# Optimization experiments

Hardware: AMD Instinct MI355X
Metric: run time of the kernel (lower is better)

## Reference

```python
import jax, jax.numpy as jnp
import numpy as np

DIM = 1024
HEADS = 16
DIM_HEAD = 64
INNER = HEADS * DIM_HEAD  # 1024
SCALE = DIM_HEAD ** -0.5


def setup_inputs() -> dict:
    key = jax.random.key(0)
    ks = jax.random.split(key, 5)
    B, N = 4, 2048
    x = jax.random.normal(ks[0], (B, N, DIM), dtype=jnp.float32)
    # torch Linear weights are [out, in]; store transposed [in, out] for x @ W
    s = 1.0 / np.sqrt(DIM)
    Wq = jax.random.uniform(ks[1], (DIM, INNER), minval=-s, maxval=s, dtype=jnp.float32)
    Wkv = jax.random.uniform(ks[2], (DIM, 2 * INNER), minval=-s, maxval=s, dtype=jnp.float32)
    so = 1.0 / np.sqrt(INNER)
    Wo = jax.random.uniform(ks[3], (INNER, DIM), minval=-so, maxval=so, dtype=jnp.float32)
    bo = jax.random.uniform(ks[4], (DIM,), minval=-so, maxval=so, dtype=jnp.float32)
    return {"x": x, "Wq": Wq, "Wkv": Wkv, "Wo": Wo, "bo": bo}


def reference(x, Wq, Wkv, Wo, bo):
    B, N, _ = x.shape
    q = x @ Wq                      # [B, N, INNER]
    kv = x @ Wkv                    # [B, N, 2*INNER]
    k, v = jnp.split(kv, 2, axis=-1)

    def split_heads(t):
        return t.reshape(B, N, HEADS, DIM_HEAD).transpose(0, 2, 1, 3)  # [B,H,N,D]

    q, k, v = split_heads(q) * SCALE, split_heads(k), split_heads(v)
    sim = jnp.einsum('bhid,bhjd->bhij', q, k)  # [B,H,N,N]
    mask_value = -jnp.finfo(sim.dtype).max
    # causal: mask strictly-upper triangle (triu with offset j-i+1 = 1)
    causal_mask = jnp.triu(jnp.ones((N, N), dtype=bool), k=1)
    sim = jnp.where(causal_mask[None, None, :, :], mask_value, sim)
    attn = jax.nn.softmax(sim, axis=-1)
    out = jnp.einsum('bhij,bhjd->bhid', attn, v)            # [B,H,N,D]
    out = out.transpose(0, 2, 1, 3).reshape(B, N, INNER)    # [B,N,INNER]
    return out @ Wo + bo
```

## Files before the change

kernel.cpp:

```cpp
#include <hip/hip_runtime.h>

typedef unsigned short u16;
typedef __bf16 bf16x8 __attribute__((ext_vector_type(8)));
typedef float floatx4 __attribute__((ext_vector_type(4)));
typedef unsigned as1_u32 __attribute__((address_space(1)));
typedef unsigned as3_u32 __attribute__((address_space(3)));

__device__ inline u16 f2bf(float f) {
    unsigned int u = __builtin_bit_cast(unsigned int, f);
    u += 0x7fffu + ((u >> 16) & 1u);
    return (u16)(u >> 16);
}
__device__ inline floatx4 mfma16(bf16x8 a, bf16x8 b, floatx4 c) {
    return __builtin_amdgcn_mfma_f32_16x16x32_bf16(a, b, c, 0, 0, 0);
}
__device__ inline void gld16(const u16* g, u16* l) {
    __builtin_amdgcn_global_load_lds((const as1_u32*)g, (as3_u32*)l, 16, 0, 0);
}
__device__ inline unsigned permpack(float lo, float hi) {
    return __builtin_amdgcn_perm(__builtin_bit_cast(unsigned, hi),
                                 __builtin_bit_cast(unsigned, lo), 0x07060302u);
}

#define NSEQ 2048
#define DIM  1024
#define HEADS 16
#define DHEAD 64
#define QSCALE 0.18033688f
#define CSHIFT 4.328085f

__device__ inline void transpose_tile(const float* __restrict__ src,
                                      u16* __restrict__ dst, int ncols,
                                      int n0, int k0, int t) {
    __shared__ u16 tile[64][72];
    #pragma unroll
    for (int rr = 0; rr < 4; rr++) {
        const int k = (t >> 4) + rr * 16;
        const int n = (t & 15) * 4;
        float4 v = *(const float4*)&src[(size_t)(k0 + k) * ncols + n0 + n];
        tile[n + 0][k] = f2bf(v.x); tile[n + 1][k] = f2bf(v.y);
        tile[n + 2][k] = f2bf(v.z); tile[n + 3][k] = f2bf(v.w);
    }
    __syncthreads();
    #pragma unroll
    for (int ww = 0; ww < 2; ww++) {
        const int idx = t + ww * 256;
        const int n = idx >> 3, g = idx & 7;
        u16 tmp[8] __attribute__((aligned(16)));
        #pragma unroll
        for (int i = 0; i < 8; i++) tmp[i] = tile[n][g * 8 + i];
        *(uint4*)&dst[(size_t)(n0 + n) * 1024 + k0 + g * 8] = *(const uint4*)tmp;
    }
}

__global__ __launch_bounds__(256) void prep_fused(
    const float* __restrict__ x,  u16* __restrict__ xb,
    const float* __restrict__ Wq, const float* __restrict__ Wkv,
    u16* __restrict__ Wt)
{
    const int bid = blockIdx.x;
    const int t = threadIdx.x;
    if (bid < 4096) {
        const size_t i = ((size_t)bid * 256 + t) * 8;
        float4 a = *(const float4*)&x[i];
        float4 b = *(const float4*)&x[i + 4];
        u16 o[8] __attribute__((aligned(16)));
        o[0] = f2bf(a.x); o[1] = f2bf(a.y); o[2] = f2bf(a.z); o[3] = f2bf(a.w);
        o[4] = f2bf(b.x); o[5] = f2bf(b.y); o[6] = f2bf(b.z); o[7] = f2bf(b.w);
        *(uint4*)&xb[i] = *(const uint4*)o;
    } else if (bid < 4352) {
        const int v = bid - 4096;
        transpose_tile(Wq, Wt, 1024, (v & 15) * 64, (v >> 4) * 64, t);
    } else {
        const int v = bid - 4352;
        transpose_tile(Wkv, Wt + (size_t)1024 * 1024, 2048, (v & 31) * 64, (v >> 5) * 64, t);
    }
}

__global__ __launch_bounds__(256) void transpose_conv(const float* __restrict__ src,
                                                      u16* __restrict__ dst, int ncols) {
    transpose_tile(src, dst, ncols, blockIdx.x * 64, blockIdx.y * 64, threadIdx.x);
}

__global__ __launch_bounds__(512, 2) void qkv_gemm_v4(
    const u16* __restrict__ xb, const u16* __restrict__ Wt,
    u16* __restrict__ q_ws, u16* __restrict__ k_ws, u16* __restrict__ v_ws)
{
    __shared__ u16 As[3][256 * 64];
    __shared__ u16 Bs[3][128 * 64];

    const int n0 = blockIdx.x * 128;
    const int m0 = blockIdx.y * 256;
    const int t = threadIdx.x, lane = t & 63, w = t >> 6;
    const int wr = w >> 1, wc = w & 1;
    const int quad = lane >> 4, l16 = lane & 15;

    const int srow = lane >> 3;
    const int c8   = (lane & 7) ^ srow;
    const size_t gA = (size_t)(m0 + w * 8 + srow) * DIM + c8 * 8;
    const size_t gB = (size_t)(n0 + w * 8 + srow) * DIM + c8 * 8;

    floatx4 acc[4][4];
    #pragma unroll
    for (int i = 0; i < 4; i++)
        #pragma unroll
        for (int j = 0; j < 4; j++) acc[i][j] = floatx4{0.f, 0.f, 0.f, 0.f};

#define STAGE_QKV(tt, buf) do {                                            \
    const size_t k0s = (size_t)(tt) * 64;                                  \
    u16* ab = &As[buf][w * 512];                                           \
    u16* bb = &Bs[buf][w * 512];                                           \
    gld16(&xb[gA + k0s],             ab);                                  \
    gld16(&xb[gA + k0s +  64 * DIM], ab + 4096);                           \
    gld16(&xb[gA + k0s + 128 * DIM], ab + 8192);                           \
    gld16(&xb[gA + k0s + 192 * DIM], ab + 12288);                          \
    gld16(&Wt[gB + k0s],             bb);                                  \
    gld16(&Wt[gB + k0s +  64 * DIM], bb + 4096);                           \
} while (0)

    STAGE_QKV(0, 0);
    STAGE_QKV(1, 1);

    int cur = 0, nxt = 2;
    for (int tt = 0; tt < 16; tt++) {
        __builtin_amdgcn_sched_barrier(0);
        __builtin_amdgcn_s_barrier();
        __builtin_amdgcn_sched_barrier(0);
        if (tt < 14) STAGE_QKV(tt + 2, nxt);
        __builtin_amdgcn_sched_barrier(0);
        if (tt < 14)       asm volatile("s_waitcnt vmcnt(12)" ::: "memory");
        else if (tt == 14) asm volatile("s_waitcnt vmcnt(6)"  ::: "memory");
        else               asm volatile("s_waitcnt vmcnt(0)"  ::: "memory");
        __builtin_amdgcn_sched_barrier(0);
        __builtin_amdgcn_s_barrier();
        __builtin_amdgcn_sched_barrier(0);

        const u16* al = &As[cur][0];
        const u16* bl = &Bs[cur][0];
        #pragma unroll
        for (int ks = 0; ks < 2; ks++) {
            bf16x8 af[4], bf[4];
            #pragma unroll
            for (int mi = 0; mi < 4; mi++)
                af[mi] = *(const bf16x8*)&al[(wr * 64 + mi * 16 + l16) * 64
                                             + (((ks * 4 + quad) ^ (l16 & 7)) * 8)];
            #pragma unroll
            for (int nj = 0; nj < 4; nj++)
                bf[nj] = *(const bf16x8*)&bl[(wc * 64 + nj * 16 + l16) * 64
                                             + (((ks * 4 + quad) ^ (l16 & 7)) * 8)];
            __builtin_amdgcn_s_setprio(1);
            #pragma unroll
            for (int mi = 0; mi < 4; mi++)
                #pragma unroll
                for (int nj = 0; nj < 4; nj++)
                    acc[mi][nj] = mfma16(af[mi], bf[nj], acc[mi][nj]);
            __builtin_amdgcn_s_setprio(0);
        }
        cur = (cur == 2) ? 0 : cur + 1;
        nxt = (nxt == 2) ? 0 : nxt + 1;
    }
#undef STAGE_QKV

    const int seg = n0 >> 10;
    #pragma unroll
    for (int nj = 0; nj < 4; nj++) {
        const int n  = n0 + wc * 64 + nj * 16 + l16;
        const int nn = n & 1023;
        const int h  = nn >> 6, d = nn & 63;
        #pragma unroll
        for (int mi = 0; mi < 4; mi++) {
            const int mb = m0 + wr * 64 + mi * 16 + quad * 4;
            const int b = mb >> 11, ib = mb & (NSEQ - 1);
            if (seg == 0) {
                #pragma unroll
                for (int r = 0; r < 4; r++)
                    q_ws[(((size_t)(b * HEADS + h)) * NSEQ + ib + r) * DHEAD + d] =
                        f2bf(acc[mi][nj][r] * QSCALE);
            } else if (seg == 1) {
                #pragma unroll
                for (int r = 0; r < 4; r++)
                    k_ws[(((size_t)(b * HEADS + h)) * NSEQ + ib + r) * DHEAD + d] =
                        f2bf(acc[mi][nj][r]);
            } else {
                u16 tmp[4] __attribute__((aligned(8)));
                #pragma unroll
                for (int r = 0; r < 4; r++) tmp[r] = f2bf(acc[mi][nj][r]);
                *(uint2*)&v_ws[(((size_t)(b * HEADS + h)) * DHEAD + d) * NSEQ + ib] =
                    *(const uint2*)tmp;
            }
        }
    }
}

__global__ __launch_bounds__(256) void attn_v8(
    const u16* __restrict__ q_ws, const u16* __restrict__ k_ws,
    const u16* __restrict__ v_ws, u16* __restrict__ attn_ws)
{
    __shared__ u16 kds[2][64 * 64];
    __shared__ u16 vds[2][64 * 64];
    __shared__ u16 p_lds[4 * 2048];

    const int bid = blockIdx.x;
    const int bh  = bid & 63;
    const int t16 = 15 - (bid >> 6);
    const int i0  = t16 * 128;
    const int b   = bh >> 4, h = bh & 15;

    const u16* qb = q_ws + (size_t)bh * NSEQ * DHEAD;
    const u16* kb = k_ws + (size_t)bh * NSEQ * DHEAD;
    const u16* vb = v_ws + (size_t)bh * DHEAD * NSEQ;

    const int t    = threadIdx.x;
    const int lane = t & 63, w = t >> 6;
    const int quad = lane >> 4, l16 = lane & 15;

    const int srow8 = lane >> 3;
    const int chunk = (lane & 7) ^ srow8;
    const int krow  = w * 16 + srow8;
    const size_t koff = (size_t)krow * DHEAD + chunk * 8;
    const size_t voff = (size_t)krow * NSEQ + chunk * 8;
    u16* klbase = (u16*)&kds[0][0] + w * 1024;
    u16* vlbase = (u16*)&vds[0][0] + w * 1024;
    const int sw = (l16 & 7);

    bf16x8 qf[2][2];
    #pragma unroll
    for (int rf = 0; rf < 2; rf++)
        #pragma unroll
        for (int dg = 0; dg < 2; dg++)
            qf[rf][dg] = *(const bf16x8*)&qb[(size_t)(i0 + rf * 64 + w * 16 + l16) * DHEAD
                                             + dg * 32 + quad * 8];

    floatx4 l4[2] = {floatx4{0.f,0.f,0.f,0.f}, floatx4{0.f,0.f,0.f,0.f}};
    floatx4 acc[2][4];
    #pragma unroll
    for (int rf = 0; rf < 2; rf++)
        #pragma unroll
        for (int dg = 0; dg < 4; dg++) acc[rf][dg] = floatx4{0.f, 0.f, 0.f, 0.f};

    const int jt_max = 2 * t16 + 1;

    gld16(&kb[koff],             klbase);
    gld16(&kb[koff + 8 * DHEAD], klbase + 512);
    gld16(&vb[voff],             vlbase);
    gld16(&vb[voff + 8 * NSEQ],  vlbase + 512);

    for (int jt = 0; jt <= jt_max; jt++) {
        const int cur = jt & 1;
        __syncthreads();

        if (jt < jt_max) {
            const size_t j64 = (size_t)(jt + 1) * 64;
            const int nb = (cur ^ 1) * 4096;
            gld16(&kb[j64 * DHEAD + koff],             klbase + nb);
            gld16(&kb[j64 * DHEAD + koff + 8 * DHEAD], klbase + nb + 512);
            gld16(&vb[j64 + voff],                     vlbase + nb);
            gld16(&vb[j64 + voff + 8 * NSEQ],          vlbase + nb + 512);
        }

        const u16* kl = &kds[cur][0];
        const u16* vl = &vds[cur][0];
        const int j0 = jt * 64;

        floatx4 s[2][4];
        #pragma unroll
        for (int rf = 0; rf < 2; rf++)
            #pragma unroll
            for (int g = 0; g < 4; g++)
                s[rf][g] = floatx4{-CSHIFT, -CSHIFT, -CSHIFT, -CSHIFT};
        __builtin_amdgcn_s_setprio(1);
        #pragma unroll
        for (int dg = 0; dg < 2; dg++)
            #pragma unroll
            for (int g = 0; g < 4; g++) {
                bf16x8 kf = *(const bf16x8*)&kl[(g * 16 + l16) * 64
                                                + (((dg * 4 + quad) ^ sw) * 8)];
                s[0][g] = mfma16(kf, qf[0][dg], s[0][g]);
                s[1][g] = mfma16(kf, qf[1][dg], s[1][g]);
            }
        __builtin_amdgcn_s_setprio(0);

        #pragma unroll
        for (int rf = 0; rf < 2; rf++) {
            const int imin = i0 + rf * 64 + w * 16;
            if (j0 + 63 > imin) {
                const int i = imin + l16;
                #pragma unroll
                for (int g = 0; g < 4; g++) {
                    const int jb = j0 + g * 16 + quad * 4;
                    #pragma unroll
                    for (int r = 0; r < 4; r++)
                        if (jb + r > i) s[rf][g][r] = -1e30f;
                }
            }
        }

        #pragma unroll
        for (int rf = 0; rf < 2; rf++) {
            #pragma unroll
            for (int g = 0; g < 4; g++) {
                #pragma unroll
                for (int r = 0; r < 4; r++)
                    s[rf][g][r] = __builtin_amdgcn_exp2f(s[rf][g][r]);
                l4[rf] += s[rf][g];
                uint2 pk;
                pk.x = permpack(s[rf][g][0], s[rf][g][1]);
                pk.y = permpack(s[rf][g][2], s[rf][g][3]);
                const int c = 2 * g + (quad >> 1);
                *(uint2*)&p_lds[w * 2048 + rf * 1024 + (c >> 2) * 512 + (c & 3) * 128
                                + l16 * 8 + (quad & 1) * 4] = pk;
            }
        }
        asm volatile("s_waitcnt lgkmcnt(0)" ::: "memory");

        __builtin_amdgcn_s_setprio(1);
        #pragma unroll
        for (int jg = 0; jg < 2; jg++) {
            bf16x8 pf0 = *(const bf16x8*)&p_lds[w * 2048 + jg * 512 + quad * 128 + l16 * 8];
            bf16x8 pf1 = *(const bf16x8*)&p_lds[w * 2048 + 1024 + jg * 512 + quad * 128 + l16 * 8];
            #pragma unroll
            for (int dg = 0; dg < 4; dg++) {
                bf16x8 vf = *(const bf16x8*)&vl[(dg * 16 + l16) * 64
                                                + (((jg * 4 + quad) ^ sw) * 8)];
                acc[0][dg] = mfma16(pf0, vf, acc[0][dg]);
                acc[1][dg] = mfma16(pf1, vf, acc[1][dg]);
            }
        }
        __builtin_amdgcn_s_setprio(0);
    }

    #pragma unroll
    for (int rf = 0; rf < 2; rf++) {
        float l_ln = (l4[rf][0] + l4[rf][1]) + (l4[rf][2] + l4[rf][3]);
        l_ln += __shfl_xor(l_ln, 16);
        l_ln += __shfl_xor(l_ln, 32);
        float linv[4];
        #pragma unroll
        for (int r = 0; r < 4; r++)
            linv[r] = 1.0f / __shfl(l_ln, quad * 4 + r);
        #pragma unroll
        for (int dg = 0; dg < 4; dg++)
            #pragma unroll
            for (int r = 0; r < 4; r++) {
                const float o = acc[rf][dg][r] * linv[r];
                const int i = i0 + rf * 64 + w * 16 + quad * 4 + r;
                attn_ws[(((size_t)(b * NSEQ + i)) * HEADS + h) * DHEAD + dg * 16 + l16] =
                    f2bf(o);
            }
    }
}

__global__ __launch_bounds__(256) void out_gemm_v3(
    const u16* __restrict__ attn, const u16* __restrict__ Wot,
    const float* __restrict__ bo, float* __restrict__ out)
{
    __shared__ u16 a0[128 * 32], a1[128 * 32];
    __shared__ u16 b0[128 * 32], b1[128 * 32];

    const int n0 = blockIdx.x * 128;
    const int m0 = blockIdx.y * 128;
    const int t = threadIdx.x, lane = t & 63, w = t >> 6;
    const int wr = w >> 1, wc = w & 1;
    const int quad = lane >> 4, l16 = lane & 15;
    const int lrow = lane >> 2, lk = (lane & 3) * 8;

    floatx4 acc[4][4];
    #pragma unroll
    for (int i = 0; i < 4; i++)
        #pragma unroll
        for (int j = 0; j < 4; j++) acc[i][j] = floatx4{0.f, 0.f, 0.f, 0.f};

    for (int k0 = 0; k0 < DIM; k0 += 64) {
        __syncthreads();
        #pragma unroll
        for (int hh = 0; hh < 2; hh++) {
            const int row = w * 32 + hh * 16;
            const size_t ga = (size_t)(m0 + row + lrow) * DIM + k0 + lk;
            const size_t gb = (size_t)(n0 + row + lrow) * DIM + k0 + lk;
            gld16(&attn[ga],      &a0[row * 32]);
            gld16(&attn[ga + 32], &a1[row * 32]);
            gld16(&Wot[gb],       &b0[row * 32]);
            gld16(&Wot[gb + 32],  &b1[row * 32]);
        }
        __syncthreads();

        #pragma unroll
        for (int ks = 0; ks < 2; ks++) {
            const u16* al = ks ? a1 : a0;
            const u16* bl = ks ? b1 : b0;
            bf16x8 af[4], bf[4];
            #pragma unroll
            for (int i = 0; i < 4; i++)
                af[i] = *(const bf16x8*)&al[(wr * 64 + i * 16 + l16) * 32 + quad * 8];
            #pragma unroll
            for (int j = 0; j < 4; j++)
                bf[j] = *(const bf16x8*)&bl[(wc * 64 + j * 16 + l16) * 32 + quad * 8];
            #pragma unroll
            for (int i = 0; i < 4; i++)
                #pragma unroll
                for (int j = 0; j < 4; j++)
                    acc[i][j] = mfma16(af[i], bf[j], acc[i][j]);
        }
    }

    #pragma unroll
    for (int j = 0; j < 4; j++) {
        const int n = n0 + wc * 64 + j * 16 + l16;
        const float bias = bo[n];
        #pragma unroll
        for (int i = 0; i < 4; i++) {
            #pragma unroll
            for (int r = 0; r < 4; r++) {
                const int m = m0 + wr * 64 + i * 16 + quad * 4 + r;
                out[(size_t)m * DIM + n] = acc[i][j][r] + bias;
            }
        }
    }
}

extern "C" void kernel_launch(void* const* d_in, const int* in_sizes, int n_in,
                              void* d_out, int out_size, void* d_ws, size_t ws_size,
                              hipStream_t stream) {
    const float* x   = (const float*)d_in[0];
    const float* Wq  = (const float*)d_in[1];
    const float* Wkv = (const float*)d_in[2];
    const float* Wo  = (const float*)d_in[3];
    const float* bo  = (const float*)d_in[4];

    u16* q_ws = (u16*)d_out;
    u16* xb   = (u16*)d_out + (size_t)8388608;

    u16* ws   = (u16*)d_ws;
    u16* k_ws = ws;
    u16* v_ws = ws + (size_t)8388608;
    u16* a_ws = ws + (size_t)16777216;
    u16* Wt   = a_ws;
    u16* Wot  = k_ws;

    prep_fused<<<4864, 256, 0, stream>>>(x, xb, Wq, Wkv, Wt);
    qkv_gemm_v4<<<dim3(24, 32), 512, 0, stream>>>(xb, Wt, q_ws, k_ws, v_ws);
    attn_v8<<<dim3(1024), 256, 0, stream>>>(q_ws, k_ws, v_ws, a_ws);
    transpose_conv<<<dim3(16, 16), 256, 0, stream>>>(Wo, Wot, 1024);
    out_gemm_v3<<<dim3(8, 64), 256, 0, stream>>>(a_ws, Wot, bo, (float*)d_out);
}
```

Baseline: 261.8 us.

## Swizzle QKV GEMM block order per XCD and split tile prefetch across barrier

The QKV GEMM now remaps its linear block index so that blocks landing on the same XCD (round-robin by 8) cover contiguous output tiles, which should improve L2 reuse of the x and weight tiles. It also splits each stage's global-to-LDS loads into two parts. The A-tile rows are issued before the wait, and the remaining A row plus the B tile are issued after the second barrier, with the vmcnt thresholds adjusted to match. Several sched_barriers are removed so the compiler has more freedom to schedule. This shortens the exposed wait per iteration, at the risk of reordering hazards if the vmcnt bookkeeping is wrong.

```diff
diff --git a/kernel.cpp b/kernel.cpp
--- a/kernel.cpp
+++ b/kernel.cpp
@@ -82,15 +82,18 @@
     transpose_tile(src, dst, ncols, blockIdx.x * 64, blockIdx.y * 64, threadIdx.x);
 }
 
-__global__ __launch_bounds__(512, 2) void qkv_gemm_v4(
+__global__ __launch_bounds__(512, 2) void qkv_gemm_v5(
     const u16* __restrict__ xb, const u16* __restrict__ Wt,
     u16* __restrict__ q_ws, u16* __restrict__ k_ws, u16* __restrict__ v_ws)
 {
     __shared__ u16 As[3][256 * 64];
     __shared__ u16 Bs[3][128 * 64];
 
-    const int n0 = blockIdx.x * 128;
-    const int m0 = blockIdx.y * 256;
+    const int h_lin = blockIdx.x + blockIdx.y * 24;
+    const int l_lin = (h_lin & 7) * 96 + (h_lin >> 3);
+    const int n0 = (l_lin % 24) * 128;
+    const int m0 = (l_lin / 24) * 256;
+
     const int t = threadIdx.x, lane = t & 63, w = t >> 6;
     const int wr = w >> 1, wc = w & 1;
     const int quad = lane >> 4, l16 = lane & 15;
@@ -106,34 +109,35 @@
         #pragma unroll
         for (int j = 0; j < 4; j++) acc[i][j] = floatx4{0.f, 0.f, 0.f, 0.f};
 
-#define STAGE_QKV(tt, buf) do {                                            \
+#define STAGE_A3(tt, buf) do {                                             \
+    const size_t k0s = (size_t)(tt) * 64;                                  \
+    u16* ab = &As[buf][w * 512];                                           \
+    gld16(&xb[gA + k0s],             ab);                                  \
+    gld16(&xb[gA + k0s +  64 * DIM], ab + 4096);                           \
+    gld16(&xb[gA + k0s + 128 * DIM], ab + 8192);                           \
+} while (0)
+#define STAGE_B3(tt, buf) do {                                             \
     const size_t k0s = (size_t)(tt) * 64;                                  \
     u16* ab = &As[buf][w * 512];                                           \
     u16* bb = &Bs[buf][w * 512];                                           \
-    gld16(&xb[gA + k0s],             ab);                                  \
-    gld16(&xb[gA + k0s +  64 * DIM], ab + 4096);                           \
-    gld16(&xb[gA + k0s + 128 * DIM], ab + 8192);                           \
     gld16(&xb[gA + k0s + 192 * DIM], ab + 12288);                          \
     gld16(&Wt[gB + k0s],             bb);                                  \
     gld16(&Wt[gB + k0s +  64 * DIM], bb + 4096);                           \
 } while (0)
 
-    STAGE_QKV(0, 0);
-    STAGE_QKV(1, 1);
+    STAGE_A3(0, 0); STAGE_B3(0, 0);
+    STAGE_A3(1, 1); STAGE_B3(1, 1);
 
     int cur = 0, nxt = 2;
     for (int tt = 0; tt < 16; tt++) {
         __builtin_amdgcn_sched_barrier(0);
         __builtin_amdgcn_s_barrier();
-        __builtin_amdgcn_sched_barrier(0);
-        if (tt < 14) STAGE_QKV(tt + 2, nxt);
-        __builtin_amdgcn_sched_barrier(0);
-        if (tt < 14)       asm volatile("s_waitcnt vmcnt(12)" ::: "memory");
-        else if (tt == 14) asm volatile("s_waitcnt vmcnt(6)"  ::: "memory");
-        else               asm volatile("s_waitcnt vmcnt(0)"  ::: "memory");
-        __builtin_amdgcn_sched_barrier(0);
+        if (tt < 14) STAGE_A3(tt + 2, nxt);
+        if (tt < 14)       asm volatile("s_waitcnt vmcnt(9)" ::: "memory");
+        else if (tt == 14) asm volatile("s_waitcnt vmcnt(6)" ::: "memory");
+        else               asm volatile("s_waitcnt vmcnt(0)" ::: "memory");
         __builtin_amdgcn_s_barrier();
-        __builtin_amdgcn_sched_barrier(0);
+        if (tt < 14) STAGE_B3(tt + 2, nxt);
 
         const u16* al = &As[cur][0];
         const u16* bl = &Bs[cur][0];
@@ -159,7 +163,8 @@
         cur = (cur == 2) ? 0 : cur + 1;
         nxt = (nxt == 2) ? 0 : nxt + 1;
     }
-#undef STAGE_QKV
+#undef STAGE_A3
+#undef STAGE_B3
 
     const int seg = n0 >> 10;
     #pragma unroll
@@ -438,7 +443,7 @@
     u16* Wot  = k_ws;
 
     prep_fused<<<4864, 256, 0, stream>>>(x, xb, Wq, Wkv, Wt);
-    qkv_gemm_v4<<<dim3(24, 32), 512, 0, stream>>>(xb, Wt, q_ws, k_ws, v_ws);
+    qkv_gemm_v5<<<dim3(24, 32), 512, 0, stream>>>(xb, Wt, q_ws, k_ws, v_ws);
     attn_v8<<<dim3(1024), 256, 0, stream>>>(q_ws, k_ws, v_ws, a_ws);
     transpose_conv<<<dim3(16, 16), 256, 0, stream>>>(Wo, Wot, 1024);
     out_gemm_v3<<<dim3(8, 64), 256, 0, stream>>>(a_ws, Wot, bo, (float*)d_out);
```

Result: no change. 264.8 us (+1.2%).
